# Kernel tuning notes

Measured on AMD Instinct MI355X. Metric: run time of the kernel, lower is better.

The kernel has to match this reference:

```python
import jax, jax.numpy as jnp
import numpy as np

B, S, D = 4, 1024, 1024
H = 16
DK = D // H  # 64
F = 4096
EPS = 1e-6


def layer_norm(x, gamma, beta):
    mu = jnp.mean(x, axis=-1, keepdims=True)
    var = jnp.mean(jnp.square(x - mu), axis=-1, keepdims=True)
    return (x - mu) * jax.lax.rsqrt(var + EPS) * gamma + beta


def setup_inputs() -> dict:
    key = jax.random.key(0)
    ks = jax.random.split(key, 16)
    sd = 0.02
    return {
        "x": jax.random.normal(ks[0], (B, S, D), dtype=jnp.float32),
        "Wq": jax.random.normal(ks[1], (H, D, DK), dtype=jnp.float32) * sd,
        "bq": jnp.zeros((H, DK), dtype=jnp.float32),
        "Wk": jax.random.normal(ks[2], (H, D, DK), dtype=jnp.float32) * sd,
        "bk": jnp.zeros((H, DK), dtype=jnp.float32),
        "Wv": jax.random.normal(ks[3], (H, D, DK), dtype=jnp.float32) * sd,
        "bv": jnp.zeros((H, DK), dtype=jnp.float32),
        "Wo": jax.random.normal(ks[4], (D, D), dtype=jnp.float32) * sd,
        "bo": jnp.zeros((D,), dtype=jnp.float32),
        "W1": jax.random.normal(ks[5], (D, F), dtype=jnp.float32) * sd,
        "b1": jnp.zeros((F,), dtype=jnp.float32),
        "W2": jax.random.normal(ks[6], (F, D), dtype=jnp.float32) * sd,
        "b2": jnp.zeros((D,), dtype=jnp.float32),
        "g1": jnp.ones((D,), dtype=jnp.float32),
        "be1": jnp.zeros((D,), dtype=jnp.float32),
        "g2": jnp.ones((D,), dtype=jnp.float32),
        "be2": jnp.zeros((D,), dtype=jnp.float32),
    }


def reference(x, Wq, bq, Wk, bk, Wv, bv, Wo, bo, W1, b1, W2, b2, g1, be1, g2, be2):
    # Per-head Dense projections, expressed as one batched einsum.
    # q/k/v: [B, H, S, DK]
    q = jnp.einsum('bsd,hdk->bhsk', x, Wq) + bq[:, None, :]
    k = jnp.einsum('bsd,hdk->bhsk', x, Wk) + bk[:, None, :]
    v = jnp.einsum('bsd,hdk->bhsk', x, Wv) + bv[:, None, :]
    scale = 1.0 / jnp.sqrt(jnp.float32(DK))
    scores = jnp.einsum('bhqk,bhsk->bhqs', q, k) * scale  # [B,H,S,S]
    attn = jax.nn.softmax(scores, axis=-1)
    ctx = jnp.einsum('bhqs,bhsk->bhqk', attn, v)  # [B,H,S,DK]
    # concat heads along last dim -> [B,S,D]
    ctx = jnp.transpose(ctx, (0, 2, 1, 3)).reshape(B, S, D)
    mh = ctx @ Wo + bo
    # dropout is identity at inference
    h1 = layer_norm(mh + x, g1, be1)
    ffn = jax.nn.relu(h1 @ W1 + b1) @ W2 + b2
    out = layer_norm(h1 + ffn, g2, be2)
    return out
```

## Files before the change

kernel.cpp:

```cpp
#include <hip/hip_runtime.h>
#include <hip/hip_bf16.h>
#include <stdint.h>


typedef __bf16 bf16x8 __attribute__((ext_vector_type(8)));
typedef __bf16 bf16x4 __attribute__((ext_vector_type(4)));
typedef float f32x4 __attribute__((ext_vector_type(4)));

__device__ __forceinline__ f32x4 mfma16(bf16x8 a, bf16x8 b, f32x4 c) {
  return __builtin_amdgcn_mfma_f32_16x16x32_bf16(a, b, c, 0, 0, 0);
}

__device__ __forceinline__ void gload_lds16(const void* g, void* l) {
  typedef const unsigned int __attribute__((address_space(1)))* GP;
  typedef unsigned int __attribute__((address_space(3)))* LP;
  __builtin_amdgcn_global_load_lds((GP)(uintptr_t)g,
                                   (LP)(unsigned int)(uintptr_t)l, 16, 0, 0);
}

template <int EPI>
__global__ __launch_bounds__(512, 2) void gemm256(
    const __bf16* __restrict__ A, const __bf16* __restrict__ BT,
    const float* __restrict__ bias, __bf16* __restrict__ Cb,
    int M, int N, int K)
{
  __shared__ __attribute__((aligned(16))) __bf16 lds[2][2][2][8192];
  const int tid = threadIdx.x;
  const int lane = tid & 63;
  const int w = tid >> 6;
  const int l15 = lane & 15, lhi = lane >> 4;

  const int nbx = gridDim.x;
  const int nwg = nbx * gridDim.y;
  const int wid = blockIdx.y * nbx + blockIdx.x;
  const int sw = (wid & 7) * (nwg >> 3) + (wid >> 3);
  const int n0 = (sw % nbx) * 256;
  const int m0 = (sw / nbx) * 256;

  const int mat = w >> 2, halfI = (w >> 1) & 1, sub = w & 1;
  const __bf16* srcM = mat ? BT : A;
  const long rowG = (long)((mat ? n0 : m0) + halfI * 128 + sub * 64 + (lane >> 3));
  const __bf16* gsrc =
      srcM + rowG * K + (((lane & 7) ^ ((lane >> 3) & 7)) << 3);
  const int ldst = sub * 4096 + lane * 8;

  const int owr = w >> 2, owc = w & 3;

  const f32x4 fz = {0.f, 0.f, 0.f, 0.f};
  f32x4 acc[8][4];
#pragma unroll
  for (int i = 0; i < 8; i++)
#pragma unroll
    for (int j = 0; j < 4; j++) acc[i][j] = fz;

  const int KT = K >> 6;
  const int swz = (l15 & 7);

#pragma unroll
  for (int i = 0; i < 8; i++)
    gload_lds16(gsrc + (long)i * 8 * K, &lds[0][mat][halfI][ldst + i * 512]);

  for (int kt = 0; kt < KT; ++kt) {
    const int buf = kt & 1;
    if (kt + 1 < KT) {
#pragma unroll
      for (int i = 0; i < 8; i++)
        gload_lds16(gsrc + (long)(kt + 1) * 64 + (long)i * 8 * K,
                    &lds[buf ^ 1][mat][halfI][ldst + i * 512]);
      asm volatile("s_waitcnt vmcnt(8)" ::: "memory");
    } else {
      asm volatile("s_waitcnt vmcnt(0)" ::: "memory");
    }
    __builtin_amdgcn_s_barrier();
    __builtin_amdgcn_sched_barrier(0);

    const __bf16* Abase = &lds[buf][0][owr][0];
    const __bf16* Bbase = &lds[buf][1][owc >> 1][0];
    const int brow0 = (owc & 1) * 64;

    bf16x8 bfr[4][2];
#pragma unroll
    for (int nf = 0; nf < 4; nf++)
#pragma unroll
      for (int kk = 0; kk < 2; kk++) {
        const int row = brow0 + nf * 16 + l15;
        bfr[nf][kk] =
            *(const bf16x8*)&Bbase[row * 64 + ((((kk << 2) | lhi) ^ swz) << 3)];
      }

#pragma unroll
    for (int q = 0; q < 4; q++) {
      bf16x8 af[2][2];
#pragma unroll
      for (int m2 = 0; m2 < 2; m2++)
#pragma unroll
        for (int kk = 0; kk < 2; kk++) {
          const int row = (q * 2 + m2) * 16 + l15;
          af[m2][kk] =
              *(const bf16x8*)&Abase[row * 64 + ((((kk << 2) | lhi) ^ swz) << 3)];
        }
      __builtin_amdgcn_s_barrier();
      __builtin_amdgcn_s_setprio(1);
#pragma unroll
      for (int m2 = 0; m2 < 2; m2++)
#pragma unroll
        for (int nf = 0; nf < 4; nf++)
#pragma unroll
          for (int kk = 0; kk < 2; kk++)
            acc[q * 2 + m2][nf] =
                mfma16(af[m2][kk], bfr[nf][kk], acc[q * 2 + m2][nf]);
      __builtin_amdgcn_s_setprio(0);
      __builtin_amdgcn_s_barrier();
    }
  }

  if (EPI == 0) {
#pragma unroll
    for (int mi = 0; mi < 8; mi++) {
      const int mB = m0 + owr * 128 + mi * 16 + lhi * 4;
#pragma unroll
      for (int nf = 0; nf < 4; nf++) {
        const int n = n0 + owc * 64 + nf * 16 + l15;
        const int proj = n >> 10, hh = (n >> 6) & 15, dk = n & 63;
        const float bs = bias[n];
#pragma unroll
        for (int rr = 0; rr < 4; rr++) {
          const int m = mB + rr;
          const int b = m >> 10, sidx = m & 1023;
          Cb[(long)proj * 4194304 +
             ((long)(b * 16 + hh) * 1024 + sidx) * 64 + dk] =
              (__bf16)(acc[mi][nf][rr] + bs);
        }
      }
    }
  } else {
#pragma unroll
    for (int mi = 0; mi < 8; mi++) {
      const int mB = m0 + owr * 128 + mi * 16 + lhi * 4;
#pragma unroll
      for (int nf = 0; nf < 4; nf++) {
        const int n = n0 + owc * 64 + nf * 16 + l15;
        const float bs = bias[n];
#pragma unroll
        for (int rr = 0; rr < 4; rr++) {
          float v = acc[mi][nf][rr] + bs;
          v = v > 0.f ? v : 0.f;
          Cb[(long)(mB + rr) * N + n] = (__bf16)v;
        }
      }
    }
  }
}

__global__ __launch_bounds__(512, 2) void gemm_ksplit(
    const __bf16* __restrict__ A, const __bf16* __restrict__ BT,
    const float* __restrict__ bias, float* __restrict__ Cf0,
    float* __restrict__ Cf1, int M, int N, int ld, int Kh)
{
  __shared__ __attribute__((aligned(16))) __bf16 As[2][8192];
  __shared__ __attribute__((aligned(16))) __bf16 Bs[2][16384];
  const int tid = threadIdx.x;
  const int lane = tid & 63;
  const int w = tid >> 6;
  const int l15 = lane & 15, lhi = lane >> 4;

  const int nbx = gridDim.x;
  const int nby = gridDim.y;
  const int nxy = nbx * nby;
  const int nwg = nxy * 2;
  const int wid = (blockIdx.z * nby + blockIdx.y) * nbx + blockIdx.x;
  const int sw = (wid & 7) * (nwg >> 3) + (wid >> 3);
  const int z = sw / nxy;
  const int rem = sw % nxy;
  const int m0 = (rem / nbx) * 128;
  const int n0 = (rem % nbx) * 256;
  const long zoff = (long)z * Kh;

  const int trow = tid >> 3;
  const int sswz = ((tid & 7) ^ (trow & 7)) << 3;
  const __bf16* gA = A + (long)(m0 + trow) * ld + zoff + sswz;
  const __bf16* gB = BT + (long)(n0 + trow) * ld + zoff + sswz;
  const int ldst = tid * 8;

  const int owr = w >> 2, owc = w & 3;

  const f32x4 fz = {0.f, 0.f, 0.f, 0.f};
  f32x4 acc[4][4];
#pragma unroll
  for (int i = 0; i < 4; i++)
#pragma unroll
    for (int j = 0; j < 4; j++) acc[i][j] = fz;

  const int KT = Kh >> 6;
  const int swz = (l15 & 7);

  {
    gload_lds16(gA, &As[0][ldst]);
    gload_lds16(gA + 64 * (long)ld, &As[0][ldst + 4096]);
    gload_lds16(gB, &Bs[0][ldst]);
    gload_lds16(gB + 64 * (long)ld, &Bs[0][ldst + 4096]);
    gload_lds16(gB + 128 * (long)ld, &Bs[0][ldst + 8192]);
    gload_lds16(gB + 192 * (long)ld, &Bs[0][ldst + 12288]);
  }

  for (int kt = 0; kt < KT; ++kt) {
    const int buf = kt & 1;
    if (kt + 1 < KT) {
      const __bf16* a0 = gA + (kt + 1) * 64;
      const __bf16* b0 = gB + (kt + 1) * 64;
      gload_lds16(a0, &As[buf ^ 1][ldst]);
      gload_lds16(a0 + 64 * (long)ld, &As[buf ^ 1][ldst + 4096]);
      gload_lds16(b0, &Bs[buf ^ 1][ldst]);
      gload_lds16(b0 + 64 * (long)ld, &Bs[buf ^ 1][ldst + 4096]);
      gload_lds16(b0 + 128 * (long)ld, &Bs[buf ^ 1][ldst + 8192]);
      gload_lds16(b0 + 192 * (long)ld, &Bs[buf ^ 1][ldst + 12288]);
      asm volatile("s_waitcnt vmcnt(6)" ::: "memory");
    } else {
      asm volatile("s_waitcnt vmcnt(0)" ::: "memory");
    }
    __builtin_amdgcn_s_barrier();
    __builtin_amdgcn_sched_barrier(0);

    const __bf16* Abase = &As[buf][owr * 4096];
    const __bf16* Bbase = &Bs[buf][owc * 4096];

    bf16x8 bfr[4][2];
#pragma unroll
    for (int nf = 0; nf < 4; nf++)
#pragma unroll
      for (int kk = 0; kk < 2; kk++) {
        const int row = nf * 16 + l15;
        bfr[nf][kk] =
            *(const bf16x8*)&Bbase[row * 64 + ((((kk << 2) | lhi) ^ swz) << 3)];
      }

#pragma unroll
    for (int q = 0; q < 4; q++) {
      bf16x8 af[2];
#pragma unroll
      for (int kk = 0; kk < 2; kk++) {
        const int row = q * 16 + l15;
        af[kk] =
            *(const bf16x8*)&Abase[row * 64 + ((((kk << 2) | lhi) ^ swz) << 3)];
      }
      __builtin_amdgcn_s_barrier();
      __builtin_amdgcn_s_setprio(1);
#pragma unroll
      for (int nf = 0; nf < 4; nf++)
#pragma unroll
        for (int kk = 0; kk < 2; kk++)
          acc[q][nf] = mfma16(af[kk], bfr[nf][kk], acc[q][nf]);
      __builtin_amdgcn_s_setprio(0);
      __builtin_amdgcn_s_barrier();
    }
  }

  float* Cf = z ? Cf1 : Cf0;
#pragma unroll
  for (int mi = 0; mi < 4; mi++) {
    const int mB = m0 + owr * 64 + mi * 16 + lhi * 4;
#pragma unroll
    for (int nf = 0; nf < 4; nf++) {
      const int n = n0 + owc * 64 + nf * 16 + l15;
      const float bs = z ? 0.f : bias[n];
#pragma unroll
      for (int rr = 0; rr < 4; rr++)
        Cf[(long)(mB + rr) * N + n] = acc[mi][nf][rr] + bs;
    }
  }
}

__global__ __launch_bounds__(256) void vtrans_kernel(
    const __bf16* __restrict__ in, __bf16* __restrict__ out)
{
  __shared__ __bf16 t[64][66];
  const int bh = blockIdx.y, s0 = blockIdx.x * 64;
  const int tx = threadIdx.x & 63, ty = threadIdx.x >> 6;
  const __bf16* ip = in + (long)bh * 65536 + (long)s0 * 64;
  __bf16* op = out + (long)bh * 65536;
#pragma unroll
  for (int i = 0; i < 64; i += 4) t[ty + i][tx] = ip[(ty + i) * 64 + tx];
  __syncthreads();
#pragma unroll
  for (int i = 0; i < 64; i += 4)
    op[(long)(ty + i) * 1024 + s0 + tx] = t[tx][ty + i];
}

__global__ __launch_bounds__(256, 2) void attn_kernel(
    const __bf16* __restrict__ qg_, const __bf16* __restrict__ kg_,
    const __bf16* __restrict__ vtg_, __bf16* __restrict__ ctx)
{
  __shared__ __attribute__((aligned(16))) __bf16 Kb[2][64 * 64];
  __shared__ __attribute__((aligned(16))) __bf16 Vb[2][64 * 64];
  __shared__ __attribute__((aligned(16))) __bf16 Ps[4][16 * 64];
  const int tid = threadIdx.x, lane = tid & 63, w = tid >> 6;
  const int l15 = lane & 15, lhi = lane >> 4;
  const int bh = blockIdx.y;
  const int b = bh >> 4, h = bh & 15;
  const int q0 = blockIdx.x * 64 + w * 16;

  const __bf16* qg = qg_ + ((long)bh * 1024 + q0) * 64;
  const __bf16* kg = kg_ + (long)bh * 65536;
  const __bf16* vtg = vtg_ + (long)bh * 65536;

  bf16x8 qa[2];
  qa[0] = *(const bf16x8*)&qg[l15 * 64 + lhi * 8];
  qa[1] = *(const bf16x8*)&qg[l15 * 64 + 32 + lhi * 8];

  const int srow0 = tid >> 3;
  const int srow1 = srow0 + 32;
  const int sw0 = (tid & 7) ^ (srow0 & 7);
  const int sw1 = (tid & 7) ^ (srow1 & 7);
  const __bf16* kst0 = kg + srow0 * 64 + sw0 * 8;
  const __bf16* kst1 = kg + srow1 * 64 + sw1 * 8;
  const __bf16* vst0 = vtg + srow0 * 1024 + sw0 * 8;
  const __bf16* vst1 = vtg + srow1 * 1024 + sw1 * 8;

  const f32x4 fz = {0.f, 0.f, 0.f, 0.f};
  float mrun[4], lrun[4];
  f32x4 o[4];
#pragma unroll
  for (int r = 0; r < 4; r++) { mrun[r] = -1e30f; lrun[r] = 0.f; }
#pragma unroll
  for (int n = 0; n < 4; n++) o[n] = fz;

  const int e = l15 & 7;
  const int c0 = (lhi ^ e) * 8;
  const int c1 = ((4 | lhi) ^ e) * 8;

  {
    __bf16* kb = &Kb[0][tid * 8];
    __bf16* vb = &Vb[0][tid * 8];
    gload_lds16(kst0, kb);
    gload_lds16(kst1, kb + 2048);
    gload_lds16(vst0, vb);
    gload_lds16(vst1, vb + 2048);
  }

  int cur = 0;
  for (int t = 0; t < 16; ++t) {
    __syncthreads();
    if (t + 1 < 16) {
      __bf16* kb = &Kb[cur ^ 1][tid * 8];
      __bf16* vb = &Vb[cur ^ 1][tid * 8];
      gload_lds16(kst0 + (t + 1) * 4096, kb);
      gload_lds16(kst1 + (t + 1) * 4096, kb + 2048);
      gload_lds16(vst0 + (t + 1) * 64, vb);
      gload_lds16(vst1 + (t + 1) * 64, vb + 2048);
    }

    f32x4 s[4];
#pragma unroll
    for (int n = 0; n < 4; n++) s[n] = fz;
    __builtin_amdgcn_s_setprio(1);
#pragma unroll
    for (int n = 0; n < 4; n++) {
      const int row = (n * 16 + l15) * 64;
      bf16x8 kb0 = *(const bf16x8*)&Kb[cur][row + c0];
      bf16x8 kb1 = *(const bf16x8*)&Kb[cur][row + c1];
      s[n] = mfma16(qa[0], kb0, s[n]);
      s[n] = mfma16(qa[1], kb1, s[n]);
    }
    __builtin_amdgcn_s_setprio(0);

    float alpha[4];
    float p[4][4];
#pragma unroll
    for (int r = 0; r < 4; r++) {
      float mx = -1e30f;
#pragma unroll
      for (int n = 0; n < 4; n++) {
        s[n][r] *= 0.125f;
        mx = fmaxf(mx, s[n][r]);
      }
#pragma unroll
      for (int off = 8; off; off >>= 1) mx = fmaxf(mx, __shfl_xor(mx, off));
      const float mnew = fmaxf(mrun[r], mx);
      alpha[r] = __expf(mrun[r] - mnew);
      float ps = 0.f;
#pragma unroll
      for (int n = 0; n < 4; n++) {
        const float pv = __expf(s[n][r] - mnew);
        p[n][r] = pv;
        ps += pv;
      }
#pragma unroll
      for (int off = 8; off; off >>= 1) ps += __shfl_xor(ps, off);
      mrun[r] = mnew;
      lrun[r] = lrun[r] * alpha[r] + ps;
    }
#pragma unroll
    for (int n = 0; n < 4; n++)
#pragma unroll
      for (int r = 0; r < 4; r++) o[n][r] *= alpha[r];

#pragma unroll
    for (int n = 0; n < 4; n++) {
      const int ch = n * 2 + (l15 >> 3);
#pragma unroll
      for (int r = 0; r < 4; r++) {
        const int row = lhi * 4 + r;
        Ps[w][row * 64 + (ch ^ (row & 7)) * 8 + e] = (__bf16)p[n][r];
      }
    }
    asm volatile("s_waitcnt lgkmcnt(0)" ::: "memory");

    __builtin_amdgcn_s_setprio(1);
#pragma unroll
    for (int kk = 0; kk < 2; kk++) {
      bf16x8 pa = *(const bf16x8*)&Ps[w][l15 * 64 + (kk ? c1 : c0)];
#pragma unroll
      for (int n = 0; n < 4; n++) {
        bf16x8 vb =
            *(const bf16x8*)&Vb[cur][(n * 16 + l15) * 64 + (kk ? c1 : c0)];
        o[n] = mfma16(pa, vb, o[n]);
      }
    }
    __builtin_amdgcn_s_setprio(0);
    cur ^= 1;
  }

  const long crow = (long)b * 1024 + q0;
#pragma unroll
  for (int n = 0; n < 4; n++)
#pragma unroll
    for (int r = 0; r < 4; r++) {
      const float val = o[n][r] / lrun[r];
      ctx[(crow + lhi * 4 + r) * 1024 + h * 64 + n * 16 + l15] = (__bf16)val;
    }
}

template <int CB, int OB>
__global__ __launch_bounds__(256) void ln_fuse3(
    const float* __restrict__ a, const float* __restrict__ b,
    const void* __restrict__ c_, const float* __restrict__ gamma,
    const float* __restrict__ beta, float* __restrict__ outf,
    __bf16* __restrict__ outb)
{
  const int row = blockIdx.x;
  const int tid = threadIdx.x;
  const float4 va = ((const float4*)(a + (long)row * 1024))[tid];
  const float4 vb = ((const float4*)(b + (long)row * 1024))[tid];
  float c0, c1, c2, c3;
  if (CB) {
    const bf16x4 cv =
        *(const bf16x4*)((const __bf16*)c_ + (long)row * 1024 + tid * 4);
    c0 = (float)cv[0]; c1 = (float)cv[1]; c2 = (float)cv[2]; c3 = (float)cv[3];
  } else {
    const float4 vc = ((const float4*)((const float*)c_ + (long)row * 1024))[tid];
    c0 = vc.x; c1 = vc.y; c2 = vc.z; c3 = vc.w;
  }
  const float x0 = va.x + vb.x + c0, x1 = va.y + vb.y + c1,
              x2 = va.z + vb.z + c2, x3 = va.w + vb.w + c3;
  float sum = x0 + x1 + x2 + x3;
  float sq = x0 * x0 + x1 * x1 + x2 * x2 + x3 * x3;
#pragma unroll
  for (int off = 32; off; off >>= 1) {
    sum += __shfl_down(sum, off);
    sq += __shfl_down(sq, off);
  }
  __shared__ float red[8];
  const int w = tid >> 6;
  if ((tid & 63) == 0) { red[w] = sum; red[4 + w] = sq; }
  __syncthreads();
  sum = red[0] + red[1] + red[2] + red[3];
  sq = red[4] + red[5] + red[6] + red[7];
  const float mean = sum * (1.f / 1024.f);
  const float var = sq * (1.f / 1024.f) - mean * mean;
  const float inv = rsqrtf(var + 1e-6f);
  const float4 g = ((const float4*)gamma)[tid];
  const float4 be = ((const float4*)beta)[tid];
  const float y0 = (x0 - mean) * inv * g.x + be.x;
  const float y1 = (x1 - mean) * inv * g.y + be.y;
  const float y2 = (x2 - mean) * inv * g.z + be.z;
  const float y3 = (x3 - mean) * inv * g.w + be.w;
  if (OB) {
    __bf16* ob = outb + (long)row * 1024 + tid * 4;
    ob[0] = (__bf16)y0; ob[1] = (__bf16)y1;
    ob[2] = (__bf16)y2; ob[3] = (__bf16)y3;
  } else {
    float4 o4; o4.x = y0; o4.y = y1; o4.z = y2; o4.w = y3;
    ((float4*)(outf + (long)row * 1024))[tid] = o4;
  }
}

__global__ __launch_bounds__(256) void cast_bf16_kernel(
    const float* __restrict__ in, __bf16* __restrict__ out, int n4)
{
  const int i = blockIdx.x * 256 + threadIdx.x;
  if (i < n4) {
    const float4 v = ((const float4*)in)[i];
    __bf16* o = out + (long)i * 4;
    o[0] = (__bf16)v.x; o[1] = (__bf16)v.y;
    o[2] = (__bf16)v.z; o[3] = (__bf16)v.w;
  }
}

__global__ __launch_bounds__(256) void pack_bias_kernel(
    const float* __restrict__ bq, const float* __restrict__ bk,
    const float* __restrict__ bv, float* __restrict__ out)
{
  const int i = blockIdx.x * 256 + threadIdx.x;
  if (i < 3072) {
    const float* src = i < 1024 ? bq : (i < 2048 ? bk : bv);
    out[i] = src[i & 1023];
  }
}

__global__ __launch_bounds__(256) void transpose_cast_kernel(
    const float* __restrict__ in, __bf16* __restrict__ out, int R, int C,
    long ibs, long obs)
{
  __shared__ float t[32][33];
  const float* ip = in + (long)blockIdx.z * ibs;
  __bf16* op = out + (long)blockIdx.z * obs;
  const int c0 = blockIdx.x * 32, r0 = blockIdx.y * 32;
  const int tx = threadIdx.x & 31, ty = threadIdx.x >> 5;
#pragma unroll
  for (int i = 0; i < 32; i += 8)
    t[ty + i][tx] = ip[(long)(r0 + ty + i) * C + (c0 + tx)];
  __syncthreads();
#pragma unroll
  for (int i = 0; i < 32; i += 8)
    op[(long)(c0 + ty + i) * R + (r0 + tx)] = (__bf16)t[tx][ty + i];
}

extern "C" void kernel_launch(void* const* d_in, const int* in_sizes, int n_in,
                              void* d_out, int out_size, void* d_ws,
                              size_t ws_size, hipStream_t stream)
{
  const float* x   = (const float*)d_in[0];
  const float* Wq  = (const float*)d_in[1];
  const float* bq  = (const float*)d_in[2];
  const float* Wk  = (const float*)d_in[3];
  const float* bk  = (const float*)d_in[4];
  const float* Wv  = (const float*)d_in[5];
  const float* bv  = (const float*)d_in[6];
  const float* Wo  = (const float*)d_in[7];
  const float* bo  = (const float*)d_in[8];
  const float* W1  = (const float*)d_in[9];
  const float* b1  = (const float*)d_in[10];
  const float* W2  = (const float*)d_in[11];
  const float* b2  = (const float*)d_in[12];
  const float* g1  = (const float*)d_in[13];
  const float* be1 = (const float*)d_in[14];
  const float* g2  = (const float*)d_in[15];
  const float* be2 = (const float*)d_in[16];
  float* out = (float*)d_out;

  char* ws = (char*)d_ws;
  __bf16* wqkvT = (__bf16*)(ws);
  __bf16* woT   = (__bf16*)(ws + 6291456);
  __bf16* w1T   = (__bf16*)(ws + 8388608);
  __bf16* w2T   = (__bf16*)(ws + 16777216);
  float*  bqkv  = (float*)(ws + 25165824);
  __bf16* xbf   = (__bf16*)(ws + 25178112);
  __bf16* ctxb  = xbf;
  __bf16* qkv   = (__bf16*)(ws + 33566720);
  float*  mh_p1 = (float*)(ws + 33566720);
  __bf16* h1b   = (__bf16*)(ws + 50343936);
  __bf16* f1b   = (__bf16*)(ws + 58732544);
  float*  f2_p1 = (float*)(ws + 25178112);
  __bf16* vt    = (__bf16*)d_out;
  float*  mh_p0 = out;
  float*  f2_p0 = out;

  cast_bf16_kernel<<<4096, 256, 0, stream>>>(x, xbf, 1048576);
  pack_bias_kernel<<<12, 256, 0, stream>>>(bq, bk, bv, bqkv);
  transpose_cast_kernel<<<dim3(2, 32, 16), 256, 0, stream>>>(
      Wq, wqkvT, 1024, 64, 65536, 65536);
  transpose_cast_kernel<<<dim3(2, 32, 16), 256, 0, stream>>>(
      Wk, wqkvT + 1048576, 1024, 64, 65536, 65536);
  transpose_cast_kernel<<<dim3(2, 32, 16), 256, 0, stream>>>(
      Wv, wqkvT + 2097152, 1024, 64, 65536, 65536);
  transpose_cast_kernel<<<dim3(32, 32, 1), 256, 0, stream>>>(
      Wo, woT, 1024, 1024, 0, 0);
  transpose_cast_kernel<<<dim3(128, 32, 1), 256, 0, stream>>>(
      W1, w1T, 1024, 4096, 0, 0);
  transpose_cast_kernel<<<dim3(32, 128, 1), 256, 0, stream>>>(
      W2, w2T, 4096, 1024, 0, 0);

  gemm256<0><<<dim3(12, 16), 512, 0, stream>>>(
      xbf, wqkvT, bqkv, qkv, 4096, 3072, 1024);

  vtrans_kernel<<<dim3(16, 64), 256, 0, stream>>>(qkv + 8388608, vt);

  attn_kernel<<<dim3(16, 64), 256, 0, stream>>>(
      qkv, qkv + 4194304, vt, ctxb);

  gemm_ksplit<<<dim3(4, 32, 2), 512, 0, stream>>>(
      ctxb, woT, bo, mh_p0, mh_p1, 4096, 1024, 1024, 512);

  ln_fuse3<0, 1><<<4096, 256, 0, stream>>>(
      mh_p0, mh_p1, x, g1, be1, nullptr, h1b);

  gemm256<1><<<dim3(16, 16), 512, 0, stream>>>(
      h1b, w1T, b1, f1b, 4096, 4096, 1024);

  gemm_ksplit<<<dim3(4, 32, 2), 512, 0, stream>>>(
      f1b, w2T, b2, f2_p0, f2_p1, 4096, 1024, 4096, 2048);

  ln_fuse3<1, 0><<<4096, 256, 0, stream>>>(
      f2_p0, f2_p1, h1b, g2, be2, out, nullptr);
}
```

Before: 358.2 us.

## Widen attention KV tile to 128 and defer softmax rescaling

```diff
diff --git a/kernel.cpp b/kernel.cpp
--- a/kernel.cpp
+++ b/kernel.cpp
@@ -290,9 +290,9 @@
     const __bf16* __restrict__ qg_, const __bf16* __restrict__ kg_,
     const __bf16* __restrict__ vtg_, __bf16* __restrict__ ctx)
 {
-  __shared__ __attribute__((aligned(16))) __bf16 Kb[2][64 * 64];
-  __shared__ __attribute__((aligned(16))) __bf16 Vb[2][64 * 64];
-  __shared__ __attribute__((aligned(16))) __bf16 Ps[4][16 * 64];
+  __shared__ __attribute__((aligned(16))) __bf16 Kb[2][8192];
+  __shared__ __attribute__((aligned(16))) __bf16 Vb[2][8192];
+  __shared__ __attribute__((aligned(16))) __bf16 Ps[4][2048];
   const int tid = threadIdx.x, lane = tid & 63, w = tid >> 6;
   const int l15 = lane & 15, lhi = lane >> 4;
   const int bh = blockIdx.y;
@@ -307,14 +307,10 @@
   qa[0] = *(const bf16x8*)&qg[l15 * 64 + lhi * 8];
   qa[1] = *(const bf16x8*)&qg[l15 * 64 + 32 + lhi * 8];
 
-  const int srow0 = tid >> 3;
-  const int srow1 = srow0 + 32;
-  const int sw0 = (tid & 7) ^ (srow0 & 7);
-  const int sw1 = (tid & 7) ^ (srow1 & 7);
-  const __bf16* kst0 = kg + srow0 * 64 + sw0 * 8;
-  const __bf16* kst1 = kg + srow1 * 64 + sw1 * 8;
-  const __bf16* vst0 = vtg + srow0 * 1024 + sw0 * 8;
-  const __bf16* vst1 = vtg + srow1 * 1024 + sw1 * 8;
+  const int krow = tid >> 3;
+  const __bf16* kst = kg + krow * 64 + (((tid & 7) ^ (krow & 7)) << 3);
+  const int vrow = tid >> 4;
+  const __bf16* vst = vtg + vrow * 1024 + (((tid & 15) ^ (vrow & 7)) << 3);
 
   const f32x4 fz = {0.f, 0.f, 0.f, 0.f};
   float mrun[4], lrun[4];
@@ -325,94 +321,100 @@
   for (int n = 0; n < 4; n++) o[n] = fz;
 
   const int e = l15 & 7;
-  const int c0 = (lhi ^ e) * 8;
-  const int c1 = ((4 | lhi) ^ e) * 8;
-
-  {
-    __bf16* kb = &Kb[0][tid * 8];
-    __bf16* vb = &Vb[0][tid * 8];
-    gload_lds16(kst0, kb);
-    gload_lds16(kst1, kb + 2048);
-    gload_lds16(vst0, vb);
-    gload_lds16(vst1, vb + 2048);
+  const float csc = 0.18033688f;
+
+#pragma unroll
+  for (int i = 0; i < 4; i++) {
+    gload_lds16(kst + i * 2048, &Kb[0][tid * 8 + i * 2048]);
+    gload_lds16(vst + i * 16384, &Vb[0][tid * 8 + i * 2048]);
   }
 
   int cur = 0;
-  for (int t = 0; t < 16; ++t) {
+  for (int t = 0; t < 8; ++t) {
     __syncthreads();
-    if (t + 1 < 16) {
-      __bf16* kb = &Kb[cur ^ 1][tid * 8];
-      __bf16* vb = &Vb[cur ^ 1][tid * 8];
-      gload_lds16(kst0 + (t + 1) * 4096, kb);
-      gload_lds16(kst1 + (t + 1) * 4096, kb + 2048);
-      gload_lds16(vst0 + (t + 1) * 64, vb);
-      gload_lds16(vst1 + (t + 1) * 64, vb + 2048);
-    }
-
-    f32x4 s[4];
-#pragma unroll
-    for (int n = 0; n < 4; n++) s[n] = fz;
+    if (t + 1 < 8) {
+#pragma unroll
+      for (int i = 0; i < 4; i++) {
+        gload_lds16(kst + (t + 1) * 8192 + i * 2048,
+                    &Kb[cur ^ 1][tid * 8 + i * 2048]);
+        gload_lds16(vst + (t + 1) * 128 + i * 16384,
+                    &Vb[cur ^ 1][tid * 8 + i * 2048]);
+      }
+    }
+
+    f32x4 s[8];
+#pragma unroll
+    for (int n = 0; n < 8; n++) s[n] = fz;
     __builtin_amdgcn_s_setprio(1);
 #pragma unroll
-    for (int n = 0; n < 4; n++) {
+    for (int n = 0; n < 8; n++) {
       const int row = (n * 16 + l15) * 64;
-      bf16x8 kb0 = *(const bf16x8*)&Kb[cur][row + c0];
-      bf16x8 kb1 = *(const bf16x8*)&Kb[cur][row + c1];
+      bf16x8 kb0 = *(const bf16x8*)&Kb[cur][row + ((lhi ^ e) << 3)];
+      bf16x8 kb1 = *(const bf16x8*)&Kb[cur][row + (((4 | lhi) ^ e) << 3)];
       s[n] = mfma16(qa[0], kb0, s[n]);
       s[n] = mfma16(qa[1], kb1, s[n]);
     }
     __builtin_amdgcn_s_setprio(0);
 
-    float alpha[4];
-    float p[4][4];
+    float mx[4];
 #pragma unroll
     for (int r = 0; r < 4; r++) {
-      float mx = -1e30f;
-#pragma unroll
-      for (int n = 0; n < 4; n++) {
-        s[n][r] *= 0.125f;
-        mx = fmaxf(mx, s[n][r]);
-      }
-#pragma unroll
-      for (int off = 8; off; off >>= 1) mx = fmaxf(mx, __shfl_xor(mx, off));
-      const float mnew = fmaxf(mrun[r], mx);
-      alpha[r] = __expf(mrun[r] - mnew);
+      float m = s[0][r];
+#pragma unroll
+      for (int n = 1; n < 8; n++) m = fmaxf(m, s[n][r]);
+#pragma unroll
+      for (int off = 8; off; off >>= 1) m = fmaxf(m, __shfl_xor(m, off));
+      mx[r] = m;
+    }
+    bool need = false;
+#pragma unroll
+    for (int r = 0; r < 4; r++) need = need || (mx[r] > mrun[r] + 64.f);
+    if (__any(need)) {
+#pragma unroll
+      for (int r = 0; r < 4; r++) {
+        const float mnew = fmaxf(mrun[r], mx[r]);
+        const float alpha = __builtin_amdgcn_exp2f((mrun[r] - mnew) * csc);
+        mrun[r] = mnew;
+        lrun[r] *= alpha;
+#pragma unroll
+        for (int n = 0; n < 4; n++) o[n][r] *= alpha;
+      }
+    }
+    float p[8][4];
+#pragma unroll
+    for (int r = 0; r < 4; r++) {
+      const float mc = mrun[r] * csc;
       float ps = 0.f;
 #pragma unroll
-      for (int n = 0; n < 4; n++) {
-        const float pv = __expf(s[n][r] - mnew);
+      for (int n = 0; n < 8; n++) {
+        const float pv = __builtin_amdgcn_exp2f(__builtin_fmaf(s[n][r], csc, -mc));
         p[n][r] = pv;
         ps += pv;
       }
 #pragma unroll
       for (int off = 8; off; off >>= 1) ps += __shfl_xor(ps, off);
-      mrun[r] = mnew;
-      lrun[r] = lrun[r] * alpha[r] + ps;
-    }
-#pragma unroll
-    for (int n = 0; n < 4; n++)
-#pragma unroll
-      for (int r = 0; r < 4; r++) o[n][r] *= alpha[r];
-
-#pragma unroll
-    for (int n = 0; n < 4; n++) {
+      lrun[r] += ps;
+    }
+
+#pragma unroll
+    for (int n = 0; n < 8; n++) {
       const int ch = n * 2 + (l15 >> 3);
 #pragma unroll
       for (int r = 0; r < 4; r++) {
         const int row = lhi * 4 + r;
-        Ps[w][row * 64 + (ch ^ (row & 7)) * 8 + e] = (__bf16)p[n][r];
+        Ps[w][row * 128 + ((ch ^ (row & 7)) << 3) + e] = (__bf16)p[n][r];
       }
     }
     asm volatile("s_waitcnt lgkmcnt(0)" ::: "memory");
 
     __builtin_amdgcn_s_setprio(1);
 #pragma unroll
-    for (int kk = 0; kk < 2; kk++) {
-      bf16x8 pa = *(const bf16x8*)&Ps[w][l15 * 64 + (kk ? c1 : c0)];
+    for (int ks = 0; ks < 4; ks++) {
+      const int co = ((((ks << 2) | lhi) ^ e) << 3);
+      bf16x8 pa = *(const bf16x8*)&Ps[w][l15 * 128 + co];
 #pragma unroll
       for (int n = 0; n < 4; n++) {
-        bf16x8 vb =
-            *(const bf16x8*)&Vb[cur][(n * 16 + l15) * 64 + (kk ? c1 : c0)];
+        bf16x8 vb = *(const bf16x8*)&Vb[cur][(n * 16 + l15) * 128 + co];
         o[n] = mfma16(pa, vb, o[n]);
       }
     }
@@ -421,11 +423,14 @@
   }
 
   const long crow = (long)b * 1024 + q0;
+  float rl[4];
+#pragma unroll
+  for (int r = 0; r < 4; r++) rl[r] = __builtin_amdgcn_rcpf(lrun[r]);
 #pragma unroll
   for (int n = 0; n < 4; n++)
 #pragma unroll
     for (int r = 0; r < 4; r++) {
-      const float val = o[n][r] / lrun[r];
+      const float val = o[n][r] * rl[r];
       ctx[(crow + lhi * 4 + r) * 1024 + h * 64 + n * 16 + l15] = (__bf16)val;
     }
 }
```

After: 353.6 us. No clear change (-1.3%).
